# Performance work log

Hardware: AMD Instinct MI355X
Metric: run time of the kernel (lower is better)

## Reference

```python
import jax, jax.numpy as jnp
import numpy as np

N_NODES = 100000
N_HIGH = 20000
N_EDGES = 200000
D = 128
HEADS = 4
EPS = 1e-16


def setup_inputs() -> dict:
    key = jax.random.key(0)
    ks = jax.random.split(key, 9)
    s = 1.0 / np.sqrt(D)
    return {
        "n_features": jax.random.normal(ks[0], (N_NODES, D), jnp.float32),
        "W_src": jax.random.normal(ks[1], (D, HEADS * D), jnp.float32) * s,
        "W_dst": jax.random.normal(ks[2], (D, HEADS * D), jnp.float32) * s,
        "att_src": jax.random.normal(ks[3], (1, HEADS, D), jnp.float32) * s,
        "att_dst": jax.random.normal(ks[4], (1, HEADS, D), jnp.float32) * s,
        "W_high": jax.random.normal(ks[5], (D, D), jnp.float32) * s,
        "b_high": jnp.zeros((D,), jnp.float32),
        "src_idx": jax.random.randint(ks[6], (N_EDGES,), 0, N_NODES),
        "dst_idx": jax.random.randint(ks[7], (N_EDGES,), 0, N_HIGH),
    }


def reference(n_features, W_src, W_dst, att_src, att_dst, W_high, b_high, src_idx, dst_idx):
    # --- edge-wise gather of node features ---
    nn_features = n_features[src_idx]                      # [E, D]
    # --- scatter-mean to hyperedge features, gather back per edge ---
    seg_sum = jax.ops.segment_sum(nn_features, dst_idx, num_segments=N_HIGH)
    cnt = jax.ops.segment_sum(jnp.ones((src_idx.shape[0],), nn_features.dtype), dst_idx, num_segments=N_HIGH)
    h_mean = seg_sum / jnp.maximum(cnt, 1.0)[:, None]       # [H, D]
    h_high_e = h_mean[dst_idx]                              # [E, D]
    # --- per-edge multi-head projections ---
    E = src_idx.shape[0]
    h_node = (nn_features @ W_src).reshape(E, HEADS, D)     # [E, h, D]
    h_high = (h_high_e @ W_dst).reshape(E, HEADS, D)        # [E, h, D]
    # --- attention scores ---
    alpha_src = (h_high * att_src).sum(-1)                  # [E, h]
    alpha_dst = (h_node * att_dst).sum(-1)                  # [E, h]
    alpha = jax.nn.leaky_relu(alpha_src + alpha_dst, 0.2)
    # --- segment softmax over edges grouped by hyperedge id ---
    amax = jax.ops.segment_max(alpha, dst_idx, num_segments=N_HIGH)
    alpha = jnp.exp(alpha - amax[dst_idx])
    asum = jax.ops.segment_sum(alpha, dst_idx, num_segments=N_HIGH)
    alpha = alpha / (asum[dst_idx] + EPS)                   # [E, h]
    # --- weight, head-mean, scatter-sum aggregate ---
    h_node = (h_node * alpha[..., None]).mean(axis=1)       # [E, D]
    h_features = jax.ops.segment_sum(h_node, dst_idx, num_segments=N_HIGH)
    h_features = h_features @ W_high + b_high               # [H, D]
    return (h_features, alpha)
```

## Files before the change

### kernel.cpp

```cpp
#include <hip/hip_runtime.h>
#include <math.h>

#define N_NODES 100000
#define N_HIGH  20000
#define N_EDGES 200000
#define D       128
#define HEADS   4
#define EPSF    1e-16f

typedef __attribute__((ext_vector_type(8))) short bf16x8;
typedef __attribute__((ext_vector_type(4))) float f32x4;
typedef unsigned short ushort_t;
typedef unsigned int uint_t;

__device__ __forceinline__ ushort_t bf16_rn(float f) {
  uint_t u = __float_as_uint(f);
  u = u + 0x7FFFu + ((u >> 16) & 1u);
  return (ushort_t)(u >> 16);
}
__device__ __forceinline__ uint_t pack_bf2(float x, float y) {
  return (uint_t)bf16_rn(x) | ((uint_t)bf16_rn(y) << 16);
}
__device__ __forceinline__ float readlane_f(float v, int q) {
  return __uint_as_float(__builtin_amdgcn_readlane(__float_as_uint(v), q));
}

constexpr size_t OFF_VSRC = 0;
constexpr size_t OFF_VDST = OFF_VSRC + 512 * 4;
constexpr size_t OFF_P    = OFF_VDST + 512 * 4;
constexpr size_t OFF_ASRC = OFF_P    + 65536 * 4;
constexpr size_t OFF_ADST = OFF_ASRC + 400000 * 4;
constexpr size_t OFF_CNT  = OFF_ADST + 400000 * 4;
constexpr size_t OFF_OFFS = OFF_CNT  + 20000 * 4;
constexpr size_t OFF_FILL = OFF_OFFS + 20004 * 4;
constexpr size_t OFF_SORT = OFF_FILL + 20000 * 4;
constexpr size_t OFF_G    = OFF_SORT + 200000 * 8;
constexpr size_t OFF_NFB  = OFF_G    + 20000 * 512 * 2;

__global__ __launch_bounds__(256) void k_vp(
    const float* __restrict__ Wsrc, const float* __restrict__ Wdst,
    const float* __restrict__ att_src, const float* __restrict__ att_dst,
    const float* __restrict__ Whigh,
    float* __restrict__ v_src, float* __restrict__ v_dst,
    int* __restrict__ cnt, ushort_t* __restrict__ Pt) {
  __shared__ float red[128];
  if (blockIdx.x < 256) {
    int gid = blockIdx.x * 256 + threadIdx.x;
    if (gid < N_HIGH) cnt[gid] = 0;

    int W = blockIdx.x * 4 + (threadIdx.x >> 6);
    int lane = threadIdx.x & 63;
    int which = W >> 9;
    int idx = W & 511;
    int k = idx >> 2, h = idx & 3;
    const float* wrow = (which ? Wdst : Wsrc) + k * (HEADS * D) + h * D;
    const float* arow = (which ? att_src : att_dst) + h * D;
    float2 wv = ((const float2*)wrow)[lane];
    float2 av = ((const float2*)arow)[lane];
    float s = wv.x * av.x + wv.y * av.y;
#pragma unroll
    for (int o = 32; o; o >>= 1) s += __shfl_xor(s, o);
    if (lane == 0) {
      if (which) v_src[k * HEADS + h] = s;
      else       v_dst[k * HEADS + h] = s;
    }
  } else {
    int hk = blockIdx.x - 256;
    int h = hk >> 7, col = hk & 127;
    int d = threadIdx.x & 127, half = threadIdx.x >> 7;
    const float* ws = Wsrc + col * (HEADS * D) + h * D + half * 64;
    const float* wh = Whigh + (size_t)(half * 64) * D + d;
    float s = 0.f;
#pragma unroll 8
    for (int m = 0; m < 64; ++m) s += ws[m] * wh[(size_t)m * D];
    if (half) red[d] = s;
    __syncthreads();
    if (!half) {
      int kp = (col >> 1) * 8 + h * 2 + (col & 1);
      Pt[(size_t)d * 512 + kp] = bf16_rn(0.25f * (s + red[d]));
    }
  }
}

#define NP_BLOCKS 1563
#define H_BLOCKS  782
__global__ __launch_bounds__(256) void k_nodehist(
    const float* __restrict__ nf,
    const float* __restrict__ v_src, const float* __restrict__ v_dst,
    float4* __restrict__ a_srcn, float4* __restrict__ a_dstn,
    const int* __restrict__ dst, int* __restrict__ cnt,
    ushort_t* __restrict__ nfb) {
  __shared__ float nfT[128 * 65];
  __shared__ float4 vsf4[128];
  __shared__ float4 vdf4[128];
  __shared__ float part[8][4][64];
  int t = threadIdx.x;
  if (blockIdx.x >= NP_BLOCKS) {
    int e = (blockIdx.x - NP_BLOCKS) * 256 + t;
    if (e < N_EDGES) atomicAdd(&cnt[dst[e]], 1);
    return;
  }
  int n0 = blockIdx.x * 64;

  if (t < 128) vsf4[t] = ((const float4*)v_src)[t];
  else vdf4[t - 128] = ((const float4*)v_dst)[t - 128];

  const float4* nf4 = (const float4*)nf;
#pragma unroll
  for (int j = 0; j < 8; ++j) {
    int f4 = j * 256 + t;
    int r = f4 >> 5, c4 = f4 & 31;
    int n = n0 + r;
    if (n > N_NODES - 1) n = N_NODES - 1;
    float4 g = nf4[(size_t)n * 32 + c4];
    nfT[(c4 * 4 + 0) * 65 + r] = g.x;
    nfT[(c4 * 4 + 1) * 65 + r] = g.y;
    nfT[(c4 * 4 + 2) * 65 + r] = g.z;
    nfT[(c4 * 4 + 3) * 65 + r] = g.w;
    ushort4 hb;
    hb.x = bf16_rn(g.x); hb.y = bf16_rn(g.y);
    hb.z = bf16_rn(g.z); hb.w = bf16_rn(g.w);
    ((ushort4*)nfb)[(size_t)n * 32 + c4] = hb;
  }
  __syncthreads();

  int l = t & 63, w = t >> 6;
  float as[4] = {0.f, 0.f, 0.f, 0.f};
  float ad[4] = {0.f, 0.f, 0.f, 0.f};
#pragma unroll 8
  for (int kk = 0; kk < 32; ++kk) {
    int k = w * 32 + kk;
    float x = nfT[k * 65 + l];
    float4 s4 = vsf4[k];
    float4 d4 = vdf4[k];
    as[0] += x * s4.x; as[1] += x * s4.y; as[2] += x * s4.z; as[3] += x * s4.w;
    ad[0] += x * d4.x; ad[1] += x * d4.y; ad[2] += x * d4.z; ad[3] += x * d4.w;
  }
#pragma unroll
  for (int v = 0; v < 4; ++v) {
    part[v][w][l] = as[v];
    part[v + 4][w][l] = ad[v];
  }
  __syncthreads();

  if (t < 64) {
    int ll = t;
    if (n0 + ll < N_NODES) {
      float4 o;
      o.x = part[0][0][ll] + part[0][1][ll] + part[0][2][ll] + part[0][3][ll];
      o.y = part[1][0][ll] + part[1][1][ll] + part[1][2][ll] + part[1][3][ll];
      o.z = part[2][0][ll] + part[2][1][ll] + part[2][2][ll] + part[2][3][ll];
      o.w = part[3][0][ll] + part[3][1][ll] + part[3][2][ll] + part[3][3][ll];
      a_srcn[n0 + ll] = o;
    }
  } else if (t < 128) {
    int ll = t - 64;
    if (n0 + ll < N_NODES) {
      float4 o;
      o.x = part[4][0][ll] + part[4][1][ll] + part[4][2][ll] + part[4][3][ll];
      o.y = part[5][0][ll] + part[5][1][ll] + part[5][2][ll] + part[5][3][ll];
      o.z = part[6][0][ll] + part[6][1][ll] + part[6][2][ll] + part[6][3][ll];
      o.w = part[7][0][ll] + part[7][1][ll] + part[7][2][ll] + part[7][3][ll];
      a_dstn[n0 + ll] = o;
    }
  }
}

#define SCAN_PER 20
__global__ __launch_bounds__(1024) void k_scan(
    const int* __restrict__ cnt, int* __restrict__ offs) {
  __shared__ int sm[1024];
  int t = threadIdx.x;
  int base = t * SCAN_PER;
  int s = 0;
  for (int i = 0; i < SCAN_PER; ++i) {
    int idx = base + i;
    s += (idx < N_HIGH) ? cnt[idx] : 0;
  }
  sm[t] = s;
  __syncthreads();
  for (int o = 1; o < 1024; o <<= 1) {
    int v = (t >= o) ? sm[t - o] : 0;
    __syncthreads();
    if (t >= o) sm[t] += v;
    __syncthreads();
  }
  int run = (t > 0) ? sm[t - 1] : 0;
  for (int i = 0; i < SCAN_PER; ++i) {
    int idx = base + i;
    if (idx < N_HIGH) {
      offs[idx] = run;
      run += cnt[idx];
    }
  }
  if (t == 1023) offs[N_HIGH] = sm[1023];
}

__global__ void k_scatter(const int* __restrict__ dst, const int* __restrict__ src,
                          const int* __restrict__ offs,
                          int* __restrict__ cnt, int2* __restrict__ sorted) {
  int e = blockIdx.x * blockDim.x + threadIdx.x;
  if (e < N_EDGES) {
    int d = dst[e];
    int pos = offs[d] + (atomicSub(&cnt[d], 1) - 1);
    sorted[pos] = make_int2(e, src[e]);
  }
}

#define RS 520
__global__ __launch_bounds__(256) void k_mg(
    const ushort_t* __restrict__ nfb,
    const float4* __restrict__ a_srcn, const float4* __restrict__ a_dstn,
    const int* __restrict__ offs, const int2* __restrict__ sorted,
    const ushort_t* __restrict__ Pt, const float* __restrict__ b,
    float* __restrict__ alpha_out, float* __restrict__ out) {
  __shared__ ushort_t Gl[16 * RS];
  int t = threadIdx.x;
  int w = t >> 6, lane = t & 63;
  int j0 = blockIdx.x * 16;

  for (int jj = 0; jj < 4; ++jj) {
    int row = w * 4 + jj;
    int j = j0 + row;
    int o0 = offs[j], o1 = offs[j + 1];
    int deg = o1 - o0;
    float2 acc[4];
#pragma unroll
    for (int h = 0; h < 4; ++h) acc[h] = make_float2(0.f, 0.f);

    if (deg > 0 && deg <= 64) {
      bool act = lane < deg;
      int2 es = sorted[o0 + (act ? lane : 0)];
      int e = es.x, sreg = es.y;
      float4 as = make_float4(0.f, 0.f, 0.f, 0.f);
      float4 ad = make_float4(0.f, 0.f, 0.f, 0.f);
      if (act) { as = a_srcn[sreg]; ad = a_dstn[sreg]; }

      float s[4] = {as.x, as.y, as.z, as.w};
#pragma unroll
      for (int o = 32; o; o >>= 1)
#pragma unroll
        for (int h = 0; h < 4; ++h) s[h] += __shfl_xor(s[h], o);
      float invdeg = 1.0f / (float)deg;
      float p[4];
      p[0] = s[0] * invdeg + ad.x;
      p[1] = s[1] * invdeg + ad.y;
      p[2] = s[2] * invdeg + ad.z;
      p[3] = s[3] * invdeg + ad.w;
      float ex[4];
#pragma unroll
      for (int h = 0; h < 4; ++h) {
        p[h] = p[h] >= 0.f ? p[h] : 0.2f * p[h];
        ex[h] = act ? expf(p[h]) : 0.f;
      }
      float se[4] = {ex[0], ex[1], ex[2], ex[3]};
#pragma unroll
      for (int o = 32; o; o >>= 1)
#pragma unroll
        for (int h = 0; h < 4; ++h) se[h] += __shfl_xor(se[h], o);
      float al[4];
#pragma unroll
      for (int h = 0; h < 4; ++h) al[h] = ex[h] / (se[h] + EPSF);
      if (act)
        ((float4*)alpha_out)[e] = make_float4(al[0], al[1], al[2], al[3]);

#pragma unroll 2
      for (int q = 0; q < deg; ++q) {
        int sq = __builtin_amdgcn_readlane(sreg, q);
        float a0 = readlane_f(al[0], q);
        float a1 = readlane_f(al[1], q);
        float a2 = readlane_f(al[2], q);
        float a3 = readlane_f(al[3], q);
        uint_t xw = ((const uint_t*)nfb)[(size_t)sq * 64 + lane];
        float xx = __uint_as_float(xw << 16);
        float xy = __uint_as_float(xw & 0xFFFF0000u);
        acc[0].x += a0 * xx; acc[0].y += a0 * xy;
        acc[1].x += a1 * xx; acc[1].y += a1 * xy;
        acc[2].x += a2 * xx; acc[2].y += a2 * xy;
        acc[3].x += a3 * xx; acc[3].y += a3 * xy;
      }
    } else if (deg > 64) {
      float s[4] = {0.f, 0.f, 0.f, 0.f};
      for (int i = lane; i < deg; i += 64) {
        int2 es = sorted[o0 + i];
        float4 a = a_srcn[es.y];
        s[0] += a.x; s[1] += a.y; s[2] += a.z; s[3] += a.w;
      }
#pragma unroll
      for (int o = 32; o; o >>= 1)
#pragma unroll
        for (int h = 0; h < 4; ++h) s[h] += __shfl_xor(s[h], o);
      float ah[4];
      float invdeg = 1.0f / (float)deg;
#pragma unroll
      for (int h = 0; h < 4; ++h) ah[h] = s[h] * invdeg;

      float se[4] = {0.f, 0.f, 0.f, 0.f};
      for (int i = lane; i < deg; i += 64) {
        int2 es = sorted[o0 + i];
        float4 a = a_dstn[es.y];
        float p[4] = {ah[0] + a.x, ah[1] + a.y, ah[2] + a.z, ah[3] + a.w};
#pragma unroll
        for (int h = 0; h < 4; ++h) {
          float pp = p[h] >= 0.f ? p[h] : 0.2f * p[h];
          se[h] += expf(pp);
        }
      }
#pragma unroll
      for (int o = 32; o; o >>= 1)
#pragma unroll
        for (int h = 0; h < 4; ++h) se[h] += __shfl_xor(se[h], o);
      float inv[4];
#pragma unroll
      for (int h = 0; h < 4; ++h) inv[h] = 1.0f / (se[h] + EPSF);

      for (int c0 = 0; c0 < deg; c0 += 64) {
        int i = c0 + lane;
        float al[4] = {0.f, 0.f, 0.f, 0.f};
        int sreg = 0;
        if (i < deg) {
          int2 es = sorted[o0 + i];
          sreg = es.y;
          float4 a = a_dstn[sreg];
          float p[4] = {ah[0] + a.x, ah[1] + a.y, ah[2] + a.z, ah[3] + a.w};
#pragma unroll
          for (int h = 0; h < 4; ++h) {
            float pp = p[h] >= 0.f ? p[h] : 0.2f * p[h];
            al[h] = expf(pp) * inv[h];
          }
          ((float4*)alpha_out)[es.x] = make_float4(al[0], al[1], al[2], al[3]);
        }
        int cl = min(64, deg - c0);
#pragma unroll 2
        for (int q = 0; q < cl; ++q) {
          int sq = __builtin_amdgcn_readlane(sreg, q);
          float a0 = readlane_f(al[0], q);
          float a1 = readlane_f(al[1], q);
          float a2 = readlane_f(al[2], q);
          float a3 = readlane_f(al[3], q);
          uint_t xw = ((const uint_t*)nfb)[(size_t)sq * 64 + lane];
          float xx = __uint_as_float(xw << 16);
          float xy = __uint_as_float(xw & 0xFFFF0000u);
          acc[0].x += a0 * xx; acc[0].y += a0 * xy;
          acc[1].x += a1 * xx; acc[1].y += a1 * xy;
          acc[2].x += a2 * xx; acc[2].y += a2 * xy;
          acc[3].x += a3 * xx; acc[3].y += a3 * xy;
        }
      }
    }
    uint4 gw;
    gw.x = pack_bf2(acc[0].x, acc[0].y);
    gw.y = pack_bf2(acc[1].x, acc[1].y);
    gw.z = pack_bf2(acc[2].x, acc[2].y);
    gw.w = pack_bf2(acc[3].x, acc[3].y);
    *(uint4*)&Gl[row * RS + lane * 8] = gw;
  }
  __syncthreads();

  int lr = lane & 15, lg = lane >> 4;
  f32x4 c0 = (f32x4){0.f, 0.f, 0.f, 0.f};
  f32x4 c1 = (f32x4){0.f, 0.f, 0.f, 0.f};
  const ushort_t* Pa = Pt + (size_t)lr * 512 + lg * 8;
  int nt0 = w * 2, nt1 = w * 2 + 1;
#pragma unroll
  for (int kt = 0; kt < 16; ++kt) {
    bf16x8 a = *(const bf16x8*)&Gl[lr * RS + kt * 32 + lg * 8];
    bf16x8 b0 = *(const bf16x8*)(Pa + (size_t)nt0 * 16 * 512 + kt * 32);
    bf16x8 b1 = *(const bf16x8*)(Pa + (size_t)nt1 * 16 * 512 + kt * 32);
    c0 = __builtin_amdgcn_mfma_f32_16x16x32_bf16(a, b0, c0, 0, 0, 0);
    c1 = __builtin_amdgcn_mfma_f32_16x16x32_bf16(a, b1, c1, 0, 0, 0);
  }
  int col0 = nt0 * 16 + lr, col1 = nt1 * 16 + lr;
  float bb0 = b[col0], bb1 = b[col1];
#pragma unroll
  for (int r = 0; r < 4; ++r) {
    int row = j0 + lg * 4 + r;
    out[(size_t)row * 128 + col0] = c0[r] + bb0;
    out[(size_t)row * 128 + col1] = c1[r] + bb1;
  }
}

extern "C" void kernel_launch(void* const* d_in, const int* in_sizes, int n_in,
                              void* d_out, int out_size, void* d_ws, size_t ws_size,
                              hipStream_t stream) {
  const float* nf      = (const float*)d_in[0];
  const float* Wsrc    = (const float*)d_in[1];
  const float* Wdst    = (const float*)d_in[2];
  const float* att_src = (const float*)d_in[3];
  const float* att_dst = (const float*)d_in[4];
  const float* Whigh   = (const float*)d_in[5];
  const float* bhigh   = (const float*)d_in[6];
  const int*   src     = (const int*)d_in[7];
  const int*   dst     = (const int*)d_in[8];

  char* ws = (char*)d_ws;
  float*    v_src  = (float*)(ws + OFF_VSRC);
  float*    v_dst  = (float*)(ws + OFF_VDST);
  ushort_t* Pt     = (ushort_t*)(ws + OFF_P);
  float4*   a_srcn = (float4*)(ws + OFF_ASRC);
  float4*   a_dstn = (float4*)(ws + OFF_ADST);
  int*      cnt    = (int*)(ws + OFF_CNT);
  int*      offs   = (int*)(ws + OFF_OFFS);
  int2*     sorted = (int2*)(ws + OFF_SORT);
  ushort_t* nfb    = (ushort_t*)(ws + OFF_NFB);

  float* out_h     = (float*)d_out;
  float* out_alpha = (float*)d_out + (size_t)N_HIGH * D;

  k_vp<<<768, 256, 0, stream>>>(Wsrc, Wdst, att_src, att_dst, Whigh,
                                v_src, v_dst, cnt, Pt);
  k_nodehist<<<NP_BLOCKS + H_BLOCKS, 256, 0, stream>>>(
      nf, v_src, v_dst, a_srcn, a_dstn, dst, cnt, nfb);
  k_scan<<<1, 1024, 0, stream>>>(cnt, offs);
  k_scatter<<<(N_EDGES + 255) / 256, 256, 0, stream>>>(dst, src, offs, cnt, sorted);
  k_mg<<<N_HIGH / 16, 256, 0, stream>>>(nfb, a_srcn, a_dstn, offs, sorted,
                                        Pt, bhigh, out_alpha, out_h);
}
```

Baseline: 119.3 us.

## Batch four hyperedges per wave in k_mg, pack node scores, warp-shuffle scan

Each wave in the aggregation kernel now handles its four hyperedges together. It issues the sorted-edge loads, node-score loads and the first eight bf16 feature rows for all four up front, then runs the reductions and accumulation in chunks of eight, so that more independent memory requests are in flight at once. The src and dst attention scores are packed into one interleaved array so both are fetched from adjacent addresses. The single-block scan drops its shared-memory Hillis-Steele loop in favour of wave shuffles plus a 16-entry wave-sum array. The cost is higher register pressure from the 4x4 accumulators and prefetched rows, which may lower occupancy.

```diff
diff --git a/kernel.cpp b/kernel.cpp
--- a/kernel.cpp
+++ b/kernel.cpp
@@ -28,9 +28,8 @@
 constexpr size_t OFF_VSRC = 0;
 constexpr size_t OFF_VDST = OFF_VSRC + 512 * 4;
 constexpr size_t OFF_P    = OFF_VDST + 512 * 4;
-constexpr size_t OFF_ASRC = OFF_P    + 65536 * 4;
-constexpr size_t OFF_ADST = OFF_ASRC + 400000 * 4;
-constexpr size_t OFF_CNT  = OFF_ADST + 400000 * 4;
+constexpr size_t OFF_APK  = OFF_P    + 65536 * 4;
+constexpr size_t OFF_CNT  = OFF_APK  + 800000 * 4;
 constexpr size_t OFF_OFFS = OFF_CNT  + 20000 * 4;
 constexpr size_t OFF_FILL = OFF_OFFS + 20004 * 4;
 constexpr size_t OFF_SORT = OFF_FILL + 20000 * 4;
@@ -87,7 +86,7 @@
 __global__ __launch_bounds__(256) void k_nodehist(
     const float* __restrict__ nf,
     const float* __restrict__ v_src, const float* __restrict__ v_dst,
-    float4* __restrict__ a_srcn, float4* __restrict__ a_dstn,
+    float4* __restrict__ a_pack,
     const int* __restrict__ dst, int* __restrict__ cnt,
     ushort_t* __restrict__ nfb) {
   __shared__ float nfT[128 * 65];
@@ -151,7 +150,7 @@
       o.y = part[1][0][ll] + part[1][1][ll] + part[1][2][ll] + part[1][3][ll];
       o.z = part[2][0][ll] + part[2][1][ll] + part[2][2][ll] + part[2][3][ll];
       o.w = part[3][0][ll] + part[3][1][ll] + part[3][2][ll] + part[3][3][ll];
-      a_srcn[n0 + ll] = o;
+      a_pack[(size_t)(n0 + ll) * 2] = o;
     }
   } else if (t < 128) {
     int ll = t - 64;
@@ -161,7 +160,7 @@
       o.y = part[5][0][ll] + part[5][1][ll] + part[5][2][ll] + part[5][3][ll];
       o.z = part[6][0][ll] + part[6][1][ll] + part[6][2][ll] + part[6][3][ll];
       o.w = part[7][0][ll] + part[7][1][ll] + part[7][2][ll] + part[7][3][ll];
-      a_dstn[n0 + ll] = o;
+      a_pack[(size_t)(n0 + ll) * 2 + 1] = o;
     }
   }
 }
@@ -169,31 +168,38 @@
 #define SCAN_PER 20
 __global__ __launch_bounds__(1024) void k_scan(
     const int* __restrict__ cnt, int* __restrict__ offs) {
-  __shared__ int sm[1024];
+  __shared__ int wsum[16];
   int t = threadIdx.x;
+  int lane = t & 63, wv = t >> 6;
   int base = t * SCAN_PER;
+  int loc[SCAN_PER];
   int s = 0;
+#pragma unroll
   for (int i = 0; i < SCAN_PER; ++i) {
     int idx = base + i;
-    s += (idx < N_HIGH) ? cnt[idx] : 0;
-  }
-  sm[t] = s;
+    loc[i] = (idx < N_HIGH) ? cnt[idx] : 0;
+    s += loc[i];
+  }
+  int tot = s;
+#pragma unroll
+  for (int o = 1; o < 64; o <<= 1) {
+    int v = __shfl_up(tot, o);
+    if (lane >= o) tot += v;
+  }
+  if (lane == 63) wsum[wv] = tot;
   __syncthreads();
-  for (int o = 1; o < 1024; o <<= 1) {
-    int v = (t >= o) ? sm[t - o] : 0;
-    __syncthreads();
-    if (t >= o) sm[t] += v;
-    __syncthreads();
-  }
-  int run = (t > 0) ? sm[t - 1] : 0;
+  int wpre = 0;
+  for (int i = 0; i < 16; ++i) wpre += (i < wv) ? wsum[i] : 0;
+  int run = wpre + tot - s;
+#pragma unroll
   for (int i = 0; i < SCAN_PER; ++i) {
     int idx = base + i;
     if (idx < N_HIGH) {
       offs[idx] = run;
-      run += cnt[idx];
-    }
-  }
-  if (t == 1023) offs[N_HIGH] = sm[1023];
+      run += loc[i];
+    }
+  }
+  if (t == 1023) offs[N_HIGH] = wpre + tot;
 }
 
 __global__ void k_scatter(const int* __restrict__ dst, const int* __restrict__ src,
@@ -210,7 +216,7 @@
 #define RS 520
 __global__ __launch_bounds__(256) void k_mg(
     const ushort_t* __restrict__ nfb,
-    const float4* __restrict__ a_srcn, const float4* __restrict__ a_dstn,
+    const float4* __restrict__ a_pack,
     const int* __restrict__ offs, const int2* __restrict__ sorted,
     const ushort_t* __restrict__ Pt, const float* __restrict__ b,
     float* __restrict__ alpha_out, float* __restrict__ out) {
@@ -218,87 +224,164 @@
   int t = threadIdx.x;
   int w = t >> 6, lane = t & 63;
   int j0 = blockIdx.x * 16;
-
-  for (int jj = 0; jj < 4; ++jj) {
-    int row = w * 4 + jj;
-    int j = j0 + row;
-    int o0 = offs[j], o1 = offs[j + 1];
-    int deg = o1 - o0;
-    float2 acc[4];
-#pragma unroll
-    for (int h = 0; h < 4; ++h) acc[h] = make_float2(0.f, 0.f);
-
-    if (deg > 0 && deg <= 64) {
-      bool act = lane < deg;
-      int2 es = sorted[o0 + (act ? lane : 0)];
-      int e = es.x, sreg = es.y;
-      float4 as = make_float4(0.f, 0.f, 0.f, 0.f);
-      float4 ad = make_float4(0.f, 0.f, 0.f, 0.f);
-      if (act) { as = a_srcn[sreg]; ad = a_dstn[sreg]; }
-
-      float s[4] = {as.x, as.y, as.z, as.w};
-#pragma unroll
-      for (int o = 32; o; o >>= 1)
-#pragma unroll
-        for (int h = 0; h < 4; ++h) s[h] += __shfl_xor(s[h], o);
-      float invdeg = 1.0f / (float)deg;
-      float p[4];
-      p[0] = s[0] * invdeg + ad.x;
-      p[1] = s[1] * invdeg + ad.y;
-      p[2] = s[2] * invdeg + ad.z;
-      p[3] = s[3] * invdeg + ad.w;
-      float ex[4];
-#pragma unroll
-      for (int h = 0; h < 4; ++h) {
-        p[h] = p[h] >= 0.f ? p[h] : 0.2f * p[h];
-        ex[h] = act ? expf(p[h]) : 0.f;
+  int jbase = j0 + w * 4;
+
+  int o[5];
+#pragma unroll
+  for (int i = 0; i < 5; ++i) o[i] = offs[jbase + i];
+  int deg[4];
+#pragma unroll
+  for (int i = 0; i < 4; ++i) deg[i] = o[i + 1] - o[i];
+
+  float2 acc[4][4];
+#pragma unroll
+  for (int i = 0; i < 4; ++i)
+#pragma unroll
+    for (int h = 0; h < 4; ++h) acc[i][h] = make_float2(0.f, 0.f);
+
+  bool fast = (deg[0] <= 64) & (deg[1] <= 64) & (deg[2] <= 64) & (deg[3] <= 64);
+  if (fast) {
+    bool act[4];
+    int e[4], sr[4];
+#pragma unroll
+    for (int i = 0; i < 4; ++i) {
+      act[i] = lane < deg[i];
+      int idx = min(o[i] + (act[i] ? lane : 0), N_EDGES - 1);
+      int2 es = sorted[idx];
+      e[i] = es.x; sr[i] = es.y;
+    }
+    const uint_t* __restrict__ nfbu = (const uint_t*)nfb;
+    uint_t x0[4][8];
+#pragma unroll
+    for (int i = 0; i < 4; ++i)
+#pragma unroll
+      for (int k = 0; k < 8; ++k) {
+        int sq = __builtin_amdgcn_readlane(sr[i], k);
+        x0[i][k] = nfbu[(size_t)sq * 64 + lane];
       }
-      float se[4] = {ex[0], ex[1], ex[2], ex[3]};
-#pragma unroll
-      for (int o = 32; o; o >>= 1)
-#pragma unroll
-        for (int h = 0; h < 4; ++h) se[h] += __shfl_xor(se[h], o);
-      float al[4];
-#pragma unroll
-      for (int h = 0; h < 4; ++h) al[h] = ex[h] / (se[h] + EPSF);
-      if (act)
-        ((float4*)alpha_out)[e] = make_float4(al[0], al[1], al[2], al[3]);
-
-#pragma unroll 2
-      for (int q = 0; q < deg; ++q) {
-        int sq = __builtin_amdgcn_readlane(sreg, q);
-        float a0 = readlane_f(al[0], q);
-        float a1 = readlane_f(al[1], q);
-        float a2 = readlane_f(al[2], q);
-        float a3 = readlane_f(al[3], q);
-        uint_t xw = ((const uint_t*)nfb)[(size_t)sq * 64 + lane];
-        float xx = __uint_as_float(xw << 16);
-        float xy = __uint_as_float(xw & 0xFFFF0000u);
-        acc[0].x += a0 * xx; acc[0].y += a0 * xy;
-        acc[1].x += a1 * xx; acc[1].y += a1 * xy;
-        acc[2].x += a2 * xx; acc[2].y += a2 * xy;
-        acc[3].x += a3 * xx; acc[3].y += a3 * xy;
+    float4 z4 = make_float4(0.f, 0.f, 0.f, 0.f);
+    float4 as[4], ad[4];
+#pragma unroll
+    for (int i = 0; i < 4; ++i) {
+      as[i] = act[i] ? a_pack[(size_t)sr[i] * 2] : z4;
+      ad[i] = act[i] ? a_pack[(size_t)sr[i] * 2 + 1] : z4;
+    }
+    float sm[4][4];
+#pragma unroll
+    for (int i = 0; i < 4; ++i) {
+      sm[i][0] = as[i].x; sm[i][1] = as[i].y;
+      sm[i][2] = as[i].z; sm[i][3] = as[i].w;
+    }
+#pragma unroll
+    for (int of = 32; of; of >>= 1)
+#pragma unroll
+      for (int i = 0; i < 4; ++i)
+#pragma unroll
+        for (int h = 0; h < 4; ++h) sm[i][h] += __shfl_xor(sm[i][h], of);
+    float al[4][4];
+    {
+      float ex[4][4];
+#pragma unroll
+      for (int i = 0; i < 4; ++i) {
+        float inv = 1.0f / (float)max(deg[i], 1);
+        float advv[4] = {ad[i].x, ad[i].y, ad[i].z, ad[i].w};
+#pragma unroll
+        for (int h = 0; h < 4; ++h) {
+          float p = sm[i][h] * inv + advv[h];
+          p = p >= 0.f ? p : 0.2f * p;
+          ex[i][h] = act[i] ? expf(p) : 0.f;
+        }
       }
-    } else if (deg > 64) {
+      float se[4][4];
+#pragma unroll
+      for (int i = 0; i < 4; ++i)
+#pragma unroll
+        for (int h = 0; h < 4; ++h) se[i][h] = ex[i][h];
+#pragma unroll
+      for (int of = 32; of; of >>= 1)
+#pragma unroll
+        for (int i = 0; i < 4; ++i)
+#pragma unroll
+          for (int h = 0; h < 4; ++h) se[i][h] += __shfl_xor(se[i][h], of);
+#pragma unroll
+      for (int i = 0; i < 4; ++i)
+#pragma unroll
+        for (int h = 0; h < 4; ++h) al[i][h] = ex[i][h] / (se[i][h] + EPSF);
+    }
+#pragma unroll
+    for (int i = 0; i < 4; ++i)
+      if (act[i])
+        ((float4*)alpha_out)[e[i]] =
+            make_float4(al[i][0], al[i][1], al[i][2], al[i][3]);
+
+#pragma unroll
+    for (int i = 0; i < 4; ++i)
+#pragma unroll
+      for (int k = 0; k < 8; ++k) {
+        float a0 = readlane_f(al[i][0], k);
+        float a1 = readlane_f(al[i][1], k);
+        float a2 = readlane_f(al[i][2], k);
+        float a3 = readlane_f(al[i][3], k);
+        float xx = __uint_as_float(x0[i][k] << 16);
+        float xy = __uint_as_float(x0[i][k] & 0xFFFF0000u);
+        acc[i][0].x += a0 * xx; acc[i][0].y += a0 * xy;
+        acc[i][1].x += a1 * xx; acc[i][1].y += a1 * xy;
+        acc[i][2].x += a2 * xx; acc[i][2].y += a2 * xy;
+        acc[i][3].x += a3 * xx; acc[i][3].y += a3 * xy;
+      }
+    int dmax = max(max(deg[0], deg[1]), max(deg[2], deg[3]));
+    int dmax8 = (dmax + 7) & ~7;
+    for (int c0 = 8; c0 < dmax8; c0 += 8) {
+      uint_t xc[4][8];
+#pragma unroll
+      for (int i = 0; i < 4; ++i)
+#pragma unroll
+        for (int k = 0; k < 8; ++k) {
+          int sq = __builtin_amdgcn_readlane(sr[i], c0 + k);
+          xc[i][k] = nfbu[(size_t)sq * 64 + lane];
+        }
+#pragma unroll
+      for (int i = 0; i < 4; ++i)
+#pragma unroll
+        for (int k = 0; k < 8; ++k) {
+          int q = c0 + k;
+          float a0 = readlane_f(al[i][0], q);
+          float a1 = readlane_f(al[i][1], q);
+          float a2 = readlane_f(al[i][2], q);
+          float a3 = readlane_f(al[i][3], q);
+          float xx = __uint_as_float(xc[i][k] << 16);
+          float xy = __uint_as_float(xc[i][k] & 0xFFFF0000u);
+          acc[i][0].x += a0 * xx; acc[i][0].y += a0 * xy;
+          acc[i][1].x += a1 * xx; acc[i][1].y += a1 * xy;
+          acc[i][2].x += a2 * xx; acc[i][2].y += a2 * xy;
+          acc[i][3].x += a3 * xx; acc[i][3].y += a3 * xy;
+        }
+    }
+  } else {
+    for (int pick = 0; pick < 4; ++pick) {
+      int o0 = o[pick];
+      int dg = deg[pick];
+      float2* ac = acc[pick];
+
       float s[4] = {0.f, 0.f, 0.f, 0.f};
-      for (int i = lane; i < deg; i += 64) {
+      for (int i = lane; i < dg; i += 64) {
         int2 es = sorted[o0 + i];
-        float4 a = a_srcn[es.y];
+        float4 a = a_pack[(size_t)es.y * 2];
         s[0] += a.x; s[1] += a.y; s[2] += a.z; s[3] += a.w;
       }
 #pragma unroll
-      for (int o = 32; o; o >>= 1)
-#pragma unroll
-        for (int h = 0; h < 4; ++h) s[h] += __shfl_xor(s[h], o);
+      for (int of = 32; of; of >>= 1)
+#pragma unroll
+        for (int h = 0; h < 4; ++h) s[h] += __shfl_xor(s[h], of);
       float ah[4];
-      float invdeg = 1.0f / (float)deg;
+      float invdeg = 1.0f / (float)max(dg, 1);
 #pragma unroll
       for (int h = 0; h < 4; ++h) ah[h] = s[h] * invdeg;
 
       float se[4] = {0.f, 0.f, 0.f, 0.f};
-      for (int i = lane; i < deg; i += 64) {
+      for (int i = lane; i < dg; i += 64) {
         int2 es = sorted[o0 + i];
-        float4 a = a_dstn[es.y];
+        float4 a = a_pack[(size_t)es.y * 2 + 1];
         float p[4] = {ah[0] + a.x, ah[1] + a.y, ah[2] + a.z, ah[3] + a.w};
 #pragma unroll
         for (int h = 0; h < 4; ++h) {
@@ -307,21 +390,21 @@
         }
       }
 #pragma unroll
-      for (int o = 32; o; o >>= 1)
-#pragma unroll
-        for (int h = 0; h < 4; ++h) se[h] += __shfl_xor(se[h], o);
+      for (int of = 32; of; of >>= 1)
+#pragma unroll
+        for (int h = 0; h < 4; ++h) se[h] += __shfl_xor(se[h], of);
       float inv[4];
 #pragma unroll
       for (int h = 0; h < 4; ++h) inv[h] = 1.0f / (se[h] + EPSF);
 
-      for (int c0 = 0; c0 < deg; c0 += 64) {
+      for (int c0 = 0; c0 < dg; c0 += 64) {
         int i = c0 + lane;
         float al[4] = {0.f, 0.f, 0.f, 0.f};
         int sreg = 0;
-        if (i < deg) {
+        if (i < dg) {
           int2 es = sorted[o0 + i];
           sreg = es.y;
-          float4 a = a_dstn[sreg];
+          float4 a = a_pack[(size_t)sreg * 2 + 1];
           float p[4] = {ah[0] + a.x, ah[1] + a.y, ah[2] + a.z, ah[3] + a.w};
 #pragma unroll
           for (int h = 0; h < 4; ++h) {
@@ -330,7 +413,7 @@
           }
           ((float4*)alpha_out)[es.x] = make_float4(al[0], al[1], al[2], al[3]);
         }
-        int cl = min(64, deg - c0);
+        int cl = min(64, dg - c0);
 #pragma unroll 2
         for (int q = 0; q < cl; ++q) {
           int sq = __builtin_amdgcn_readlane(sreg, q);
@@ -341,25 +424,28 @@
           uint_t xw = ((const uint_t*)nfb)[(size_t)sq * 64 + lane];
           float xx = __uint_as_float(xw << 16);
           float xy = __uint_as_float(xw & 0xFFFF0000u);
-          acc[0].x += a0 * xx; acc[0].y += a0 * xy;
-          acc[1].x += a1 * xx; acc[1].y += a1 * xy;
-          acc[2].x += a2 * xx; acc[2].y += a2 * xy;
-          acc[3].x += a3 * xx; acc[3].y += a3 * xy;
+          ac[0].x += a0 * xx; ac[0].y += a0 * xy;
+          ac[1].x += a1 * xx; ac[1].y += a1 * xy;
+          ac[2].x += a2 * xx; ac[2].y += a2 * xy;
+          ac[3].x += a3 * xx; ac[3].y += a3 * xy;
         }
       }
     }
+  }
+#pragma unroll
+  for (int i = 0; i < 4; ++i) {
     uint4 gw;
-    gw.x = pack_bf2(acc[0].x, acc[0].y);
-    gw.y = pack_bf2(acc[1].x, acc[1].y);
-    gw.z = pack_bf2(acc[2].x, acc[2].y);
-    gw.w = pack_bf2(acc[3].x, acc[3].y);
-    *(uint4*)&Gl[row * RS + lane * 8] = gw;
+    gw.x = pack_bf2(acc[i][0].x, acc[i][0].y);
+    gw.y = pack_bf2(acc[i][1].x, acc[i][1].y);
+    gw.z = pack_bf2(acc[i][2].x, acc[i][2].y);
+    gw.w = pack_bf2(acc[i][3].x, acc[i][3].y);
+    *(uint4*)&Gl[(w * 4 + i) * RS + lane * 8] = gw;
   }
   __syncthreads();
 
   int lr = lane & 15, lg = lane >> 4;
-  f32x4 c0 = (f32x4){0.f, 0.f, 0.f, 0.f};
-  f32x4 c1 = (f32x4){0.f, 0.f, 0.f, 0.f};
+  f32x4 c0v = (f32x4){0.f, 0.f, 0.f, 0.f};
+  f32x4 c1v = (f32x4){0.f, 0.f, 0.f, 0.f};
   const ushort_t* Pa = Pt + (size_t)lr * 512 + lg * 8;
   int nt0 = w * 2, nt1 = w * 2 + 1;
 #pragma unroll
@@ -367,16 +453,16 @@
     bf16x8 a = *(const bf16x8*)&Gl[lr * RS + kt * 32 + lg * 8];
     bf16x8 b0 = *(const bf16x8*)(Pa + (size_t)nt0 * 16 * 512 + kt * 32);
     bf16x8 b1 = *(const bf16x8*)(Pa + (size_t)nt1 * 16 * 512 + kt * 32);
-    c0 = __builtin_amdgcn_mfma_f32_16x16x32_bf16(a, b0, c0, 0, 0, 0);
-    c1 = __builtin_amdgcn_mfma_f32_16x16x32_bf16(a, b1, c1, 0, 0, 0);
+    c0v = __builtin_amdgcn_mfma_f32_16x16x32_bf16(a, b0, c0v, 0, 0, 0);
+    c1v = __builtin_amdgcn_mfma_f32_16x16x32_bf16(a, b1, c1v, 0, 0, 0);
   }
   int col0 = nt0 * 16 + lr, col1 = nt1 * 16 + lr;
   float bb0 = b[col0], bb1 = b[col1];
 #pragma unroll
   for (int r = 0; r < 4; ++r) {
     int row = j0 + lg * 4 + r;
-    out[(size_t)row * 128 + col0] = c0[r] + bb0;
-    out[(size_t)row * 128 + col1] = c1[r] + bb1;
+    out[(size_t)row * 128 + col0] = c0v[r] + bb0;
+    out[(size_t)row * 128 + col1] = c1v[r] + bb1;
   }
 }
 
@@ -397,8 +483,7 @@
   float*    v_src  = (float*)(ws + OFF_VSRC);
   float*    v_dst  = (float*)(ws + OFF_VDST);
   ushort_t* Pt     = (ushort_t*)(ws + OFF_P);
-  float4*   a_srcn = (float4*)(ws + OFF_ASRC);
-  float4*   a_dstn = (float4*)(ws + OFF_ADST);
+  float4*   a_pack = (float4*)(ws + OFF_APK);
   int*      cnt    = (int*)(ws + OFF_CNT);
   int*      offs   = (int*)(ws + OFF_OFFS);
   int2*     sorted = (int2*)(ws + OFF_SORT);
@@ -410,9 +495,10 @@
   k_vp<<<768, 256, 0, stream>>>(Wsrc, Wdst, att_src, att_dst, Whigh,
                                 v_src, v_dst, cnt, Pt);
   k_nodehist<<<NP_BLOCKS + H_BLOCKS, 256, 0, stream>>>(
-      nf, v_src, v_dst, a_srcn, a_dstn, dst, cnt, nfb);
+      nf, v_src, v_dst, a_pack, dst, cnt, nfb);
   k_scan<<<1, 1024, 0, stream>>>(cnt, offs);
-  k_scatter<<<(N_EDGES + 255) / 256, 256, 0, stream>>>(dst, src, offs, cnt, sorted);
-  k_mg<<<N_HIGH / 16, 256, 0, stream>>>(nfb, a_srcn, a_dstn, offs, sorted,
+  k_scatter<<<(N_EDGES + 255) / 256, 256, 0, stream>>>(
+      dst, src, offs, cnt, sorted);
+  k_mg<<<N_HIGH / 16, 256, 0, stream>>>(nfb, a_pack, offs, sorted,
                                         Pt, bhigh, out_alpha, out_h);
 }
```

Measured after the change: 104.5 us. 12.4% less time.
